# Performance work log

Measured on AMD Instinct MI355X. Metric: run time of the kernel, lower is better.

## Reference

```python
import jax, jax.numpy as jnp
import numpy as np

W_BIT = 4
G_SIZE = 128
HID = 4096
INTER = 11008
TOKS = (2, 2048)


def _dequant(qw, qz, scales, g_size):
    """Unpack int4 nibbles from int32 and dequantize: (w - zero) * scale.
    qw: [K, N//8] int32, qz: [K//g, N//8] int32, scales: [K//g, N] float.
    Returns dense weight [K, N] in scales.dtype."""
    K = qw.shape[0]
    shifts = (jnp.arange(8, dtype=jnp.int32) * 4)  # 8 nibbles per int32
    w = ((qw[:, :, None] >> shifts) & 0xF).reshape(K, -1).astype(scales.dtype)   # [K, N]
    z = ((qz[:, :, None] >> shifts) & 0xF).reshape(qz.shape[0], -1).astype(scales.dtype)  # [K//g, N]
    zr = jnp.repeat(z, g_size, axis=0)       # broadcast zero-points over group rows
    sr = jnp.repeat(scales, g_size, axis=0)  # broadcast scales over group rows
    return (w - zr) * sr


def setup_inputs() -> dict:
    key = jax.random.key(0)
    ks = jax.random.split(key, 7)
    B, S = TOKS
    x = jax.random.normal(ks[0], (B, S, HID), dtype=jnp.float32)
    imax = 2147483647
    qweight_gu = jax.random.randint(ks[1], (HID, 2 * INTER // 8), 0, imax, dtype=jnp.int32)
    qzeros_gu = jax.random.randint(ks[2], (HID // G_SIZE, 2 * INTER // 8), 0, imax, dtype=jnp.int32)
    scales_gu = jax.random.uniform(ks[3], (HID // G_SIZE, 2 * INTER), dtype=jnp.float32) * 0.01 + 1e-3
    qweight_dn = jax.random.randint(ks[4], (INTER, HID // 8), 0, imax, dtype=jnp.int32)
    qzeros_dn = jax.random.randint(ks[5], (INTER // G_SIZE, HID // 8), 0, imax, dtype=jnp.int32)
    scales_dn = jax.random.uniform(ks[6], (INTER // G_SIZE, HID), dtype=jnp.float32) * 0.01 + 1e-3
    return {"x": x, "qweight_gu": qweight_gu, "qzeros_gu": qzeros_gu, "scales_gu": scales_gu,
            "qweight_dn": qweight_dn, "qzeros_dn": qzeros_dn, "scales_dn": scales_dn}


def reference(x, qweight_gu, qzeros_gu, scales_gu, qweight_dn, qzeros_dn, scales_dn):
    # gate_up projection: x [B,S,H] @ W_gu [H, 2*I]
    W_gu = _dequant(qweight_gu, qzeros_gu, scales_gu, G_SIZE)
    gate_up = jnp.einsum('bsh,hi->bsi', x, W_gu)
    d = gate_up.shape[-1] // 2
    # SiluAndMul: silu(gate) * up
    h = jax.nn.silu(gate_up[..., :d]) * gate_up[..., d:]
    # down projection: h [B,S,I] @ W_dn [I, H]
    W_dn = _dequant(qweight_dn, qzeros_dn, scales_dn, G_SIZE)
    return jnp.einsum('bsi,ih->bsh', h, W_dn)
```

## Files before the change

### kernel.cpp

```cpp
#include <hip/hip_runtime.h>
#include <hip/hip_bf16.h>
#include <cstdint>
#include <cstddef>

#define AS1 __attribute__((address_space(1)))
#define AS3 __attribute__((address_space(3)))

constexpr int HIDC   = 4096;
constexpr int INTERC = 11008;
constexpr int NTOKC  = 4096;
constexpr int NWGU   = 2 * INTERC;

using f32x4 = __attribute__((ext_vector_type(4))) float;
using s16x8 = __attribute__((ext_vector_type(8))) short;

__device__ __forceinline__ short f2bf(float f) {
  __hip_bfloat16 h = __float2bfloat16(f);
  return __builtin_bit_cast(short, h);
}


__global__ void cvt_x_kernel(const float4* __restrict__ x, ushort4* __restrict__ xb, int n4) {
  int stride = gridDim.x * blockDim.x;
  for (int i = blockIdx.x * blockDim.x + threadIdx.x; i < n4; i += stride) {
    float4 v = x[i];
    ushort4 o;
    o.x = (unsigned short)f2bf(v.x);
    o.y = (unsigned short)f2bf(v.y);
    o.z = (unsigned short)f2bf(v.z);
    o.w = (unsigned short)f2bf(v.w);
    xb[i] = o;
  }
}

__global__ void repack_kernel(const uint32_t* __restrict__ qw, uint32_t* __restrict__ qt,
                              int kints, int Wn) {
  long total  = (long)Wn * kints;
  long stride = (long)gridDim.x * blockDim.x;
  for (long idx = blockIdx.x * (long)blockDim.x + threadIdx.x; idx < total; idx += stride) {
    int col = (int)(idx / kints);
    int kk  = (int)(idx - (long)col * kints);
    uint32_t ow[8] = {0, 0, 0, 0, 0, 0, 0, 0};
#pragma unroll
    for (int j = 0; j < 8; ++j) {
      uint32_t v = qw[(size_t)(kk * 8 + j) * Wn + col];
#pragma unroll
      for (int jn = 0; jn < 8; ++jn)
        ow[jn] |= ((v >> (4 * jn)) & 0xFu) << (4 * j);
    }
#pragma unroll
    for (int jn = 0; jn < 8; ++jn)
      qt[(size_t)(col * 8 + jn) * kints + kk] = ow[jn];
  }
}

__global__ void mktab_kernel(const uint32_t* __restrict__ qz, const float* __restrict__ sc,
                             float2* __restrict__ tab, int total, int Nw) {
  int stride = gridDim.x * blockDim.x;
  for (int idx = blockIdx.x * blockDim.x + threadIdx.x; idx < total; idx += stride) {
    int g = idx / Nw, n = idx - g * Nw;
    uint32_t z = (qz[(size_t)g * (Nw >> 3) + (n >> 3)] >> ((n & 7) * 4)) & 0xFu;
    float s = sc[idx];
    tab[idx] = make_float2(s, -s * (float)z);
  }
}

template <int DUAL, int KSTEPS, int KINTS, int NWTOT>
__global__ __launch_bounds__(256, 2) void qgemm_kernel(
    const __hip_bfloat16* __restrict__ A, const uint32_t* __restrict__ QT,
    const float2* __restrict__ TAB, __hip_bfloat16* __restrict__ Hout,
    float* __restrict__ Fout) {
  constexpr int K  = KSTEPS * 64;
  constexpr int NI = DUAL ? 2 : 4;
  __shared__ __align__(16) char lds[32768];

  const int tid  = threadIdx.x;
  const int lane = tid & 63;
  const int w    = tid >> 6;
  const int wr   = w >> 1, wc = w & 1;
  const int fr   = lane & 15;
  const int fq   = lane >> 4;
  const int nt   = blockIdx.x, mt = blockIdx.y;
  const int row0 = mt * 128;

  int a_src[4];
#pragma unroll
  for (int i = 0; i < 4; ++i) {
    int o = i * 4096 + tid * 16;
    int r = o >> 7;
    int b = (o & 127) ^ ((r & 7) << 4);
    a_src[i] = (row0 + r) * K + (b >> 1);
  }

  int s_mat, s_nl, s_kh, s_nglob;
  if (DUAL) {
    s_mat = tid >> 7;
    int tt = tid & 127;
    s_nl  = tt >> 1;
    s_kh  = tt & 1;
    s_nglob = nt * 64 + s_nl + (s_mat ? INTERC : 0);
  } else {
    s_mat = 0;
    s_nl  = tid >> 1;
    s_kh  = tid & 1;
    s_nglob = nt * 128 + s_nl;
  }
  char* bdst = lds + 16384 + s_mat * 8192 + s_nl * 128;
  const int bswz = (s_nl & 7) << 4;

  f32x4 acc0[4][NI] = {};
  f32x4 acc1[4][NI] = {};

#pragma unroll 1
  for (int kt = 0; kt < KSTEPS; ++kt) {
    if (kt) __syncthreads();

#pragma unroll
    for (int i = 0; i < 4; ++i) {
      const __hip_bfloat16* src = A + a_src[i] + kt * 64;
      __builtin_amdgcn_global_load_lds((const AS1 uint32_t*)src,
                                       (AS3 uint32_t*)(lds + i * 4096 + w * 1024),
                                       16, 0, 0);
    }

    {
      const int g = kt >> 1;
      const uint32_t* qp = QT + (size_t)s_nglob * KINTS + kt * 8 + s_kh * 4;
      uint4 q = *(const uint4*)qp;
      float2 sz = TAB[(size_t)g * NWTOT + s_nglob];
      uint32_t qq[4] = {q.x, q.y, q.z, q.w};
#pragma unroll
      for (int ii = 0; ii < 4; ++ii) {
        s16x8 wv;
#pragma unroll
        for (int j = 0; j < 8; ++j) {
          float v = (float)((qq[ii] >> (4 * j)) & 0xFu);
          wv[j] = f2bf(fmaf(v, sz.x, sz.y));
        }
        *(s16x8*)(bdst + ((s_kh * 64 + ii * 16) ^ bswz)) = wv;
      }
    }
    __syncthreads();

#pragma unroll
    for (int kk = 0; kk < 2; ++kk) {
      const int bb = (((kk << 2) | fq) ^ (fr & 7)) << 4;
      s16x8 av[4];
#pragma unroll
      for (int mi = 0; mi < 4; ++mi)
        av[mi] = *(const s16x8*)(lds + (wr * 64 + mi * 16 + fr) * 128 + bb);
      if (DUAL) {
#pragma unroll
        for (int ni = 0; ni < 2; ++ni) {
          const int brow = (wc * 32 + ni * 16 + fr) * 128 + bb;
          s16x8 bg = *(const s16x8*)(lds + 16384 + brow);
          s16x8 bu = *(const s16x8*)(lds + 24576 + brow);
#pragma unroll
          for (int mi = 0; mi < 4; ++mi) {
            acc0[mi][ni] = __builtin_amdgcn_mfma_f32_16x16x32_bf16(av[mi], bg, acc0[mi][ni], 0, 0, 0);
            acc1[mi][ni] = __builtin_amdgcn_mfma_f32_16x16x32_bf16(av[mi], bu, acc1[mi][ni], 0, 0, 0);
          }
        }
      } else {
#pragma unroll
        for (int ni = 0; ni < 4; ++ni) {
          s16x8 bv = *(const s16x8*)(lds + 16384 + (wc * 64 + ni * 16 + fr) * 128 + bb);
#pragma unroll
          for (int mi = 0; mi < 4; ++mi)
            acc0[mi][ni] = __builtin_amdgcn_mfma_f32_16x16x32_bf16(av[mi], bv, acc0[mi][ni], 0, 0, 0);
        }
      }
    }
  }

  if (DUAL) {
    const int col0 = nt * 64 + wc * 32;
#pragma unroll
    for (int mi = 0; mi < 4; ++mi) {
      const int rr = row0 + wr * 64 + mi * 16 + fq * 4;
#pragma unroll
      for (int ni = 0; ni < NI; ++ni) {
        const int cc = col0 + ni * 16 + fr;
#pragma unroll
        for (int r = 0; r < 4; ++r) {
          float gv = acc0[mi][ni][r];
          float uv = acc1[mi][ni][r];
          float hv = gv / (1.0f + __expf(-gv)) * uv;
          Hout[(size_t)(rr + r) * INTERC + cc] = __float2bfloat16(hv);
        }
      }
    }
  } else {
    const int col0 = nt * 128 + wc * 64;
#pragma unroll
    for (int mi = 0; mi < 4; ++mi) {
      const int rr = row0 + wr * 64 + mi * 16 + fq * 4;
#pragma unroll
      for (int ni = 0; ni < NI; ++ni) {
        const int cc = col0 + ni * 16 + fr;
#pragma unroll
        for (int r = 0; r < 4; ++r)
          Fout[(size_t)(rr + r) * HIDC + cc] = acc0[mi][ni][r];
      }
    }
  }
}

extern "C" void kernel_launch(void* const* d_in, const int* in_sizes, int n_in,
                              void* d_out, int out_size, void* d_ws, size_t ws_size,
                              hipStream_t stream) {
  const float*    x     = (const float*)d_in[0];
  const uint32_t* qw_gu = (const uint32_t*)d_in[1];
  const uint32_t* qz_gu = (const uint32_t*)d_in[2];
  const float*    sc_gu = (const float*)d_in[3];
  const uint32_t* qw_dn = (const uint32_t*)d_in[4];
  const uint32_t* qz_dn = (const uint32_t*)d_in[5];
  const float*    sc_dn = (const float*)d_in[6];
  float* out = (float*)d_out;

  char* ws = (char*)d_ws;
  __hip_bfloat16* xb   = (__hip_bfloat16*)(ws + 0);
  uint32_t*       qtgu = (uint32_t*)(ws + 33554432);
  uint32_t*       qtdn = (uint32_t*)(ws + 78643200);
  float2*         tgu  = (float2*)(ws + 101187584);
  float2*         tdn  = (float2*)(ws + 106823680);
  __hip_bfloat16* hbuf = (__hip_bfloat16*)(ws + 109641728);

  cvt_x_kernel<<<2048, 256, 0, stream>>>((const float4*)x, (ushort4*)xb, NTOKC * HIDC / 4);
  repack_kernel<<<2048, 256, 0, stream>>>(qw_gu, qtgu, HIDC / 8, NWGU / 8);
  repack_kernel<<<2048, 256, 0, stream>>>(qw_dn, qtdn, INTERC / 8, HIDC / 8);
  mktab_kernel<<<1024, 256, 0, stream>>>(qz_gu, sc_gu, tgu, (HIDC / 128) * NWGU, NWGU);
  mktab_kernel<<<1024, 256, 0, stream>>>(qz_dn, sc_dn, tdn, (INTERC / 128) * HIDC, HIDC);

  qgemm_kernel<1, 64, 512, NWGU>
      <<<dim3(INTERC / 64, NTOKC / 128), 256, 0, stream>>>(xb, qtgu, tgu, hbuf, nullptr);
  qgemm_kernel<0, 172, 1376, HIDC>
      <<<dim3(HIDC / 128, NTOKC / 128), 256, 0, stream>>>(hbuf, qtdn, tdn, nullptr, out);
}
```

Baseline: 1.323 ms.

## Rewrite int4 GEMMs with fp16 packed dequant, larger tiles and double buffering

Switches activations and dequantized weights from bf16 to fp16, so dequantization uses the magic-number 0x6400 trick with packed half2 sub and fma, with nibbles reordered during repack. The GEMM now uses 512-thread blocks computing 256x256 (down) or 256x128 (gate/up) tiles. The A and B tiles are double buffered in 128KB of LDS, and the next weight block is prefetched into registers. Blocks are remapped for L2 locality and MFMA sections get a raised wave priority. Together these aim to cut ALU dequant cost, raise operand reuse and overlap loads with compute, at the risk of fp16 overflow or precision loss and lower occupancy from heavy LDS use.

```diff
diff --git a/kernel.cpp b/kernel.cpp
--- a/kernel.cpp
+++ b/kernel.cpp
@@ -1,5 +1,6 @@
 #include <hip/hip_runtime.h>
 #include <hip/hip_bf16.h>
+#include <hip/hip_fp16.h>
 #include <cstdint>
 #include <cstddef>
 
@@ -12,24 +13,19 @@
 constexpr int NWGU   = 2 * INTERC;
 
 using f32x4 = __attribute__((ext_vector_type(4))) float;
-using s16x8 = __attribute__((ext_vector_type(8))) short;
-
-__device__ __forceinline__ short f2bf(float f) {
-  __hip_bfloat16 h = __float2bfloat16(f);
-  return __builtin_bit_cast(short, h);
-}
-
-
-__global__ void cvt_x_kernel(const float4* __restrict__ x, ushort4* __restrict__ xb, int n4) {
+using f16x8 = __attribute__((ext_vector_type(8))) _Float16;
+
+
+__global__ void cvt_x_kernel(const float4* __restrict__ x, ushort4* __restrict__ xh, int n4) {
   int stride = gridDim.x * blockDim.x;
   for (int i = blockIdx.x * blockDim.x + threadIdx.x; i < n4; i += stride) {
     float4 v = x[i];
     ushort4 o;
-    o.x = (unsigned short)f2bf(v.x);
-    o.y = (unsigned short)f2bf(v.y);
-    o.z = (unsigned short)f2bf(v.z);
-    o.w = (unsigned short)f2bf(v.w);
-    xb[i] = o;
+    o.x = __builtin_bit_cast(unsigned short, __float2half(v.x));
+    o.y = __builtin_bit_cast(unsigned short, __float2half(v.y));
+    o.z = __builtin_bit_cast(unsigned short, __float2half(v.z));
+    o.w = __builtin_bit_cast(unsigned short, __float2half(v.w));
+    xh[i] = o;
   }
 }
 
@@ -44,9 +40,10 @@
 #pragma unroll
     for (int j = 0; j < 8; ++j) {
       uint32_t v = qw[(size_t)(kk * 8 + j) * Wn + col];
+      const int pos = (j & 1) ? (4 + (j >> 1)) : (j >> 1);
 #pragma unroll
       for (int jn = 0; jn < 8; ++jn)
-        ow[jn] |= ((v >> (4 * jn)) & 0xFu) << (4 * j);
+        ow[jn] |= ((v >> (4 * jn)) & 0xFu) << (4 * pos);
     }
 #pragma unroll
     for (int jn = 0; jn < 8; ++jn)
@@ -55,152 +52,161 @@
 }
 
 __global__ void mktab_kernel(const uint32_t* __restrict__ qz, const float* __restrict__ sc,
-                             float2* __restrict__ tab, int total, int Nw) {
+                             uint2* __restrict__ tab, int total, int Nw) {
   int stride = gridDim.x * blockDim.x;
   for (int idx = blockIdx.x * blockDim.x + threadIdx.x; idx < total; idx += stride) {
     int g = idx / Nw, n = idx - g * Nw;
     uint32_t z = (qz[(size_t)g * (Nw >> 3) + (n >> 3)] >> ((n & 7) * 4)) & 0xFu;
     float s = sc[idx];
-    tab[idx] = make_float2(s, -s * (float)z);
-  }
-}
-
-template <int DUAL, int KSTEPS, int KINTS, int NWTOT>
-__global__ __launch_bounds__(256, 2) void qgemm_kernel(
-    const __hip_bfloat16* __restrict__ A, const uint32_t* __restrict__ QT,
-    const float2* __restrict__ TAB, __hip_bfloat16* __restrict__ Hout,
+    uint32_t us = (uint32_t)__builtin_bit_cast(unsigned short, __float2half(s));
+    uint32_t uc = (uint32_t)__builtin_bit_cast(unsigned short, __float2half(-s * (float)z));
+    tab[idx] = make_uint2(us | (us << 16), uc | (uc << 16));
+  }
+}
+
+template <int DUAL, int NT, int KINTS, int NWTOT, int NXT, int K>
+__global__ __launch_bounds__(512, 2) void qgemm_kernel(
+    const __half* __restrict__ A, const uint32_t* __restrict__ QT,
+    const uint2* __restrict__ TAB, __half* __restrict__ Hout,
     float* __restrict__ Fout) {
-  constexpr int K  = KSTEPS * 64;
-  constexpr int NI = DUAL ? 2 : 4;
-  __shared__ __align__(16) char lds[32768];
+  __shared__ __align__(16) char lds[131072];
 
   const int tid  = threadIdx.x;
   const int lane = tid & 63;
   const int w    = tid >> 6;
-  const int wr   = w >> 1, wc = w & 1;
+  const int wr   = w >> 2, wc = w & 3;
   const int fr   = lane & 15;
   const int fq   = lane >> 4;
-  const int nt   = blockIdx.x, mt = blockIdx.y;
-  const int row0 = mt * 128;
+
+  const int nwg8 = (int)gridDim.x >> 3;
+  const int g2   = (blockIdx.x & 7) * nwg8 + ((int)blockIdx.x >> 3);
+  const int mt   = g2 / NXT;
+  const int nt   = g2 - mt * NXT;
+  const int row0 = mt * 256;
 
   int a_src[4];
 #pragma unroll
   for (int i = 0; i < 4; ++i) {
-    int o = i * 4096 + tid * 16;
+    int o = i * 8192 + tid * 16;
     int r = o >> 7;
     int b = (o & 127) ^ ((r & 7) << 4);
     a_src[i] = (row0 + r) * K + (b >> 1);
   }
 
-  int s_mat, s_nl, s_kh, s_nglob;
+  const int tc = tid >> 1, kh = tid & 1;
+  int wcol;
   if (DUAL) {
-    s_mat = tid >> 7;
-    int tt = tid & 127;
-    s_nl  = tt >> 1;
-    s_kh  = tt & 1;
-    s_nglob = nt * 64 + s_nl + (s_mat ? INTERC : 0);
+    const int p = tc >> 5, mat = (tc >> 4) & 1, c16 = tc & 15;
+    wcol = nt * 128 + p * 16 + c16 + mat * INTERC;
   } else {
-    s_mat = 0;
-    s_nl  = tid >> 1;
-    s_kh  = tid & 1;
-    s_nglob = nt * 128 + s_nl;
-  }
-  char* bdst = lds + 16384 + s_mat * 8192 + s_nl * 128;
-  const int bswz = (s_nl & 7) << 4;
-
-  f32x4 acc0[4][NI] = {};
-  f32x4 acc1[4][NI] = {};
-
-#pragma unroll 1
-  for (int kt = 0; kt < KSTEPS; ++kt) {
-    if (kt) __syncthreads();
-
-#pragma unroll
-    for (int i = 0; i < 4; ++i) {
-      const __hip_bfloat16* src = A + a_src[i] + kt * 64;
-      __builtin_amdgcn_global_load_lds((const AS1 uint32_t*)src,
-                                       (AS3 uint32_t*)(lds + i * 4096 + w * 1024),
+    wcol = nt * 256 + tc;
+  }
+  const uint32_t* qbase = QT + (size_t)wcol * KINTS + kh * 4;
+  const int boff = 32768 + tc * 128;
+  const int bswz = (tc & 7) << 4;
+
+  f32x4 acc[8][4] = {};
+
+  auto stageA = [&](int kt, int buf) {
+#pragma unroll
+    for (int i = 0; i < 4; ++i)
+      __builtin_amdgcn_global_load_lds((const AS1 uint32_t*)(A + a_src[i] + kt * 64),
+                                       (AS3 uint32_t*)(lds + buf * 65536 + i * 8192 + w * 1024),
                                        16, 0, 0);
-    }
-
-    {
-      const int g = kt >> 1;
-      const uint32_t* qp = QT + (size_t)s_nglob * KINTS + kt * 8 + s_kh * 4;
-      uint4 q = *(const uint4*)qp;
-      float2 sz = TAB[(size_t)g * NWTOT + s_nglob];
-      uint32_t qq[4] = {q.x, q.y, q.z, q.w};
-#pragma unroll
-      for (int ii = 0; ii < 4; ++ii) {
-        s16x8 wv;
-#pragma unroll
-        for (int j = 0; j < 8; ++j) {
-          float v = (float)((qq[ii] >> (4 * j)) & 0xFu);
-          wv[j] = f2bf(fmaf(v, sz.x, sz.y));
-        }
-        *(s16x8*)(bdst + ((s_kh * 64 + ii * 16) ^ bswz)) = wv;
+  };
+
+  auto dequantB = [&](uint4 q, uint2 tz, int buf) {
+    const __half2 s2 = __builtin_bit_cast(__half2, tz.x);
+    const __half2 c2 = __builtin_bit_cast(__half2, tz.y);
+    const __half2 k1024 = __builtin_bit_cast(__half2, 0x64006400u);
+    char* bd = lds + buf * 65536 + boff;
+    uint32_t qq[4] = {q.x, q.y, q.z, q.w};
+#pragma unroll
+    for (int ii = 0; ii < 4; ++ii) {
+      uint32_t r[4];
+#pragma unroll
+      for (int i = 0; i < 4; ++i) {
+        uint32_t pr = ((qq[ii] >> (4 * i)) & 0x000F000Fu) | 0x64006400u;
+        __half2 t  = __hsub2(__builtin_bit_cast(__half2, pr), k1024);
+        __half2 wv = __hfma2(t, s2, c2);
+        r[i] = __builtin_bit_cast(uint32_t, wv);
       }
-    }
-    __syncthreads();
-
+      *(uint4*)(bd + ((kh * 64 + ii * 16) ^ bswz)) = make_uint4(r[0], r[1], r[2], r[3]);
+    }
+  };
+
+  auto compute = [&](int buf) {
+    const char* base = lds + buf * 65536;
 #pragma unroll
     for (int kk = 0; kk < 2; ++kk) {
       const int bb = (((kk << 2) | fq) ^ (fr & 7)) << 4;
-      s16x8 av[4];
-#pragma unroll
-      for (int mi = 0; mi < 4; ++mi)
-        av[mi] = *(const s16x8*)(lds + (wr * 64 + mi * 16 + fr) * 128 + bb);
-      if (DUAL) {
-#pragma unroll
-        for (int ni = 0; ni < 2; ++ni) {
-          const int brow = (wc * 32 + ni * 16 + fr) * 128 + bb;
-          s16x8 bg = *(const s16x8*)(lds + 16384 + brow);
-          s16x8 bu = *(const s16x8*)(lds + 24576 + brow);
-#pragma unroll
-          for (int mi = 0; mi < 4; ++mi) {
-            acc0[mi][ni] = __builtin_amdgcn_mfma_f32_16x16x32_bf16(av[mi], bg, acc0[mi][ni], 0, 0, 0);
-            acc1[mi][ni] = __builtin_amdgcn_mfma_f32_16x16x32_bf16(av[mi], bu, acc1[mi][ni], 0, 0, 0);
-          }
-        }
-      } else {
-#pragma unroll
-        for (int ni = 0; ni < 4; ++ni) {
-          s16x8 bv = *(const s16x8*)(lds + 16384 + (wc * 64 + ni * 16 + fr) * 128 + bb);
-#pragma unroll
-          for (int mi = 0; mi < 4; ++mi)
-            acc0[mi][ni] = __builtin_amdgcn_mfma_f32_16x16x32_bf16(av[mi], bv, acc0[mi][ni], 0, 0, 0);
+      f16x8 av[8], bv[4];
+#pragma unroll
+      for (int mi = 0; mi < 8; ++mi)
+        av[mi] = *(const f16x8*)(base + (wr * 128 + mi * 16 + fr) * 128 + bb);
+#pragma unroll
+      for (int ni = 0; ni < 4; ++ni)
+        bv[ni] = *(const f16x8*)(base + 32768 + (wc * 64 + ni * 16 + fr) * 128 + bb);
+      __builtin_amdgcn_s_setprio(1);
+#pragma unroll
+      for (int mi = 0; mi < 8; ++mi)
+#pragma unroll
+        for (int ni = 0; ni < 4; ++ni)
+          acc[mi][ni] = __builtin_amdgcn_mfma_f32_16x16x32_f16(av[mi], bv[ni], acc[mi][ni], 0, 0, 0);
+      __builtin_amdgcn_s_setprio(0);
+    }
+  };
+
+  uint4 q  = *(const uint4*)qbase;
+  uint2 tz = TAB[(size_t)wcol];
+  stageA(0, 0);
+  dequantB(q, tz, 0);
+  __syncthreads();
+  q  = *(const uint4*)(qbase + 8);
+  tz = TAB[(size_t)(1 >> 1) * NWTOT + wcol];
+
+  int cur = 0;
+#pragma unroll 1
+  for (int kt = 0; kt < NT; ++kt) {
+    if (kt + 1 < NT) {
+      stageA(kt + 1, cur ^ 1);
+      dequantB(q, tz, cur ^ 1);
+    }
+    if (kt + 2 < NT) {
+      q  = *(const uint4*)(qbase + (kt + 2) * 8);
+      tz = TAB[(size_t)((kt + 2) >> 1) * NWTOT + wcol];
+    }
+    compute(cur);
+    __syncthreads();
+    cur ^= 1;
+  }
+
+  if (DUAL) {
+#pragma unroll
+    for (int mi = 0; mi < 8; ++mi) {
+      const int rr = row0 + wr * 128 + mi * 16 + fq * 4;
+#pragma unroll
+      for (int pp = 0; pp < 2; ++pp) {
+        const int hcol = nt * 128 + (wc * 2 + pp) * 16 + fr;
+#pragma unroll
+        for (int r = 0; r < 4; ++r) {
+          float gv = acc[mi][2 * pp][r];
+          float uv = acc[mi][2 * pp + 1][r];
+          float hv = gv / (1.0f + __expf(-gv)) * uv;
+          Hout[(size_t)(rr + r) * INTERC + hcol] = __float2half(hv);
         }
       }
     }
-  }
-
-  if (DUAL) {
-    const int col0 = nt * 64 + wc * 32;
-#pragma unroll
-    for (int mi = 0; mi < 4; ++mi) {
-      const int rr = row0 + wr * 64 + mi * 16 + fq * 4;
-#pragma unroll
-      for (int ni = 0; ni < NI; ++ni) {
-        const int cc = col0 + ni * 16 + fr;
-#pragma unroll
-        for (int r = 0; r < 4; ++r) {
-          float gv = acc0[mi][ni][r];
-          float uv = acc1[mi][ni][r];
-          float hv = gv / (1.0f + __expf(-gv)) * uv;
-          Hout[(size_t)(rr + r) * INTERC + cc] = __float2bfloat16(hv);
-        }
-      }
-    }
   } else {
-    const int col0 = nt * 128 + wc * 64;
-#pragma unroll
-    for (int mi = 0; mi < 4; ++mi) {
-      const int rr = row0 + wr * 64 + mi * 16 + fq * 4;
-#pragma unroll
-      for (int ni = 0; ni < NI; ++ni) {
-        const int cc = col0 + ni * 16 + fr;
+#pragma unroll
+    for (int mi = 0; mi < 8; ++mi) {
+      const int rr = row0 + wr * 128 + mi * 16 + fq * 4;
+#pragma unroll
+      for (int ni = 0; ni < 4; ++ni) {
+        const int cc = nt * 256 + wc * 64 + ni * 16 + fr;
 #pragma unroll
         for (int r = 0; r < 4; ++r)
-          Fout[(size_t)(rr + r) * HIDC + cc] = acc0[mi][ni][r];
+          Fout[(size_t)(rr + r) * HIDC + cc] = acc[mi][ni][r];
       }
     }
   }
@@ -219,21 +225,21 @@
   float* out = (float*)d_out;
 
   char* ws = (char*)d_ws;
-  __hip_bfloat16* xb   = (__hip_bfloat16*)(ws + 0);
-  uint32_t*       qtgu = (uint32_t*)(ws + 33554432);
-  uint32_t*       qtdn = (uint32_t*)(ws + 78643200);
-  float2*         tgu  = (float2*)(ws + 101187584);
-  float2*         tdn  = (float2*)(ws + 106823680);
-  __hip_bfloat16* hbuf = (__hip_bfloat16*)(ws + 109641728);
-
-  cvt_x_kernel<<<2048, 256, 0, stream>>>((const float4*)x, (ushort4*)xb, NTOKC * HIDC / 4);
+  __half*   xh   = (__half*)(ws + 0);
+  uint32_t* qtgu = (uint32_t*)(ws + 33554432);
+  uint32_t* qtdn = (uint32_t*)(ws + 78643200);
+  uint2*    tgu  = (uint2*)(ws + 101187584);
+  uint2*    tdn  = (uint2*)(ws + 106823680);
+  __half*   hbuf = (__half*)(ws + 109641728);
+
+  cvt_x_kernel<<<2048, 256, 0, stream>>>((const float4*)x, (ushort4*)xh, NTOKC * HIDC / 4);
   repack_kernel<<<2048, 256, 0, stream>>>(qw_gu, qtgu, HIDC / 8, NWGU / 8);
   repack_kernel<<<2048, 256, 0, stream>>>(qw_dn, qtdn, INTERC / 8, HIDC / 8);
   mktab_kernel<<<1024, 256, 0, stream>>>(qz_gu, sc_gu, tgu, (HIDC / 128) * NWGU, NWGU);
   mktab_kernel<<<1024, 256, 0, stream>>>(qz_dn, sc_dn, tdn, (INTERC / 128) * HIDC, HIDC);
 
-  qgemm_kernel<1, 64, 512, NWGU>
-      <<<dim3(INTERC / 64, NTOKC / 128), 256, 0, stream>>>(xb, qtgu, tgu, hbuf, nullptr);
-  qgemm_kernel<0, 172, 1376, HIDC>
-      <<<dim3(HIDC / 128, NTOKC / 128), 256, 0, stream>>>(hbuf, qtdn, tdn, nullptr, out);
-}
+  qgemm_kernel<1, 64, 512, NWGU, 86, HIDC>
+      <<<1376, 512, 0, stream>>>(xh, qtgu, tgu, hbuf, nullptr);
+  qgemm_kernel<0, 172, 1376, HIDC, 16, INTERC>
+      <<<256, 512, 0, stream>>>(hbuf, qtdn, tdn, nullptr, out);
+}
```

Result: no change. 1.328 ms (+0.4%).
